# Kernel optimization log

Hardware: AMD Instinct MI355X
Metric: run time of the kernel (lower is better)

The kernel has to match this reference:

```python
import jax, jax.numpy as jnp
import numpy as np

B, S, D, H = 1, 3072, 2048, 16
HD = D // H          # head_dim = 128
C = HD // 2          # rotary complex pairs = 64
EPS = 1e-6
WINDOW = 3           # frames of sliding-window attention on each side
L_TOKENS = 256       # tokens per frame (forward arg L)
NUM_FRAMES = S // L_TOKENS


def setup_inputs() -> dict:
    key = jax.random.key(0)
    ks = jax.random.split(key, 5)
    scale = 1.0 / np.sqrt(D)
    x = jax.random.normal(ks[0], (B, S, D), jnp.float32)
    wq = jax.random.normal(ks[1], (D, D), jnp.float32) * scale
    wk = jax.random.normal(ks[2], (D, D), jnp.float32) * scale
    wv = jax.random.normal(ks[3], (D, D), jnp.float32) * scale
    wo = jax.random.normal(ks[4], (D, D), jnp.float32) * scale
    bq = jnp.zeros((D,), jnp.float32)
    bk = jnp.zeros((D,), jnp.float32)
    bv = jnp.zeros((D,), jnp.float32)
    bo = jnp.zeros((D,), jnp.float32)
    gq = jnp.ones((D,), jnp.float32)
    gk = jnp.ones((D,), jnp.float32)
    # rotary freqs as cos/sin of angle t * theta_c (source uses a complex [S,1,C] tensor)
    t = jnp.arange(S, dtype=jnp.float32)
    inv_freq = 1.0 / (10000.0 ** (jnp.arange(C, dtype=jnp.float32) / C))
    ang = t[:, None] * inv_freq[None, :]        # [S, C]
    cos = jnp.cos(ang)[:, None, :]              # [S, 1, C]
    sin = jnp.sin(ang)[:, None, :]              # [S, 1, C]
    return {"x": x, "wq": wq, "bq": bq, "wk": wk, "bk": bk, "wv": wv,
            "bv": bv, "wo": wo, "bo": bo, "gq": gq, "gk": gk,
            "cos": cos, "sin": sin, "f": NUM_FRAMES, "L": L_TOKENS}


def _rms_norm(h, g, eps=EPS):
    # tensor_parallel_rms_norm with tp_size=1: fp32 variance, rsqrt, scale by weight
    hf = h.astype(jnp.float32)
    var = jnp.mean(hf * hf, axis=-1, keepdims=True)
    return (hf * jax.lax.rsqrt(var + eps) * g).astype(h.dtype)


def _rope(h, cos, sin):
    # complex rotation on interleaved (real, imag) pairs per head (rope_apply_for3d)
    b, s, d = h.shape
    hd = 2 * cos.shape[-1]
    n = d // hd
    hr = h.reshape(b, s, n, hd)
    xr, xi = hr[..., 0::2], hr[..., 1::2]       # [b,s,n,C]
    c, sn = cos[None], sin[None]                # [1,s,1,C] broadcast over heads
    yr = xr * c - xi * sn
    yi = xr * sn + xi * c
    y = jnp.stack([yr, yi], axis=-1).reshape(b, s, n, hd)
    return y.reshape(b, s, d)


def reference(x, wq, bq, wk, bk, wv, bv, wo, bo, gq, gk, cos, sin, f, L):
    q = _rope(_rms_norm(x @ wq.T + bq, gq), cos, sin)
    k = _rope(_rms_norm(x @ wk.T + bk, gk), cos, sin)
    v = x @ wv.T + bv
    b, s, d = q.shape
    hd = 2 * cos.shape[-1]
    n = d // hd
    qh = q.reshape(b, s, n, hd)
    kh = k.reshape(b, s, n, hd)
    vh = v.reshape(b, s, n, hd)
    scale = 1.0 / np.sqrt(hd)
    scores = jnp.einsum('bqnd,bknd->bnqk', qh, kh) * scale
    win = L * WINDOW
    idx = jnp.arange(s)
    delta = idx[None, :] - idx[:, None]
    mask = (delta <= win) & (delta >= -win)
    scores = jnp.where(mask[None, None], scores, -jnp.inf)
    probs = jax.nn.softmax(scores, axis=-1)
    out = jnp.einsum('bnqk,bknd->bqnd', probs, vh).reshape(b, s, d)
    return out @ wo.T + bo
```

## Files before the change

kernel.cpp:

```cpp
#include <hip/hip_runtime.h>
#include <stdint.h>

typedef unsigned short u16;
typedef __attribute__((ext_vector_type(8))) short short8;
typedef __attribute__((ext_vector_type(4))) float f32x4;

#define S_LEN 3072
#define D_DIM 2048
#define WIN 768
#define INV_SQRT_HD 0.08838834764831845f
#define M_SHIFT 12.0f

__device__ __forceinline__ u16 f2bf(float x) {
  union { float f; uint32_t u; } v; v.f = x;
  uint32_t r = v.u + 0x7FFFu + ((v.u >> 16) & 1u);
  return (u16)(r >> 16);
}
__device__ __forceinline__ float bf2f(u16 x) {
  union { uint32_t u; float f; } v; v.u = ((uint32_t)x) << 16;
  return v.f;
}

__device__ __forceinline__ void load_lds16(const void* g, void* l) {
  __builtin_amdgcn_global_load_lds(
      (const __attribute__((address_space(1))) void*)g,
      (__attribute__((address_space(3))) void*)l, 16, 0, 0);
}

#define MFMA16(a, b, c) __builtin_amdgcn_mfma_f32_16x16x32_bf16((a), (b), (c), 0, 0, 0)

__global__ __launch_bounds__(256) void k_cvt_all(const float* __restrict__ x,
                                                 const float* __restrict__ w0, const float* __restrict__ w1,
                                                 const float* __restrict__ w2, const float* __restrict__ w3,
                                                 const float* __restrict__ bq, const float* __restrict__ bk,
                                                 const float* __restrict__ bv,
                                                 u16* __restrict__ xo,
                                                 u16* __restrict__ o0, u16* __restrict__ o1,
                                                 u16* __restrict__ o2, u16* __restrict__ o3,
                                                 float* __restrict__ bias_all,
                                                 int n4x, int n4w) {
  int i = blockIdx.x * 256 + threadIdx.x;
  if (i < n4x + 4 * n4w) {
    const float* in;
    u16* out;
    int off;
    if (i < n4x) {
      in = x; out = xo; off = i;
    } else {
      int j = i - n4x;
      int seg = j / n4w;
      off = j - seg * n4w;
      in = seg == 0 ? w0 : seg == 1 ? w1 : seg == 2 ? w2 : w3;
      out = seg == 0 ? o0 : seg == 1 ? o1 : seg == 2 ? o2 : o3;
    }
    float4 v = ((const float4*)in)[off];
    ushort4 o;
    o.x = f2bf(v.x); o.y = f2bf(v.y); o.z = f2bf(v.z); o.w = f2bf(v.w);
    ((ushort4*)out)[off] = o;
  } else {
    int j = i - n4x - 4 * n4w;
    int seg = j >> 9, off = j & 511;
    const float* in = seg == 0 ? bq : seg == 1 ? bk : bv;
    ((float4*)bias_all)[j] = ((const float4*)in)[off];
  }
}

__global__ __launch_bounds__(256, 3) void k_gemm_qkv(const u16* __restrict__ A,
                                                     const u16* __restrict__ Ball,
                                                     const float* __restrict__ bias_all,
                                                     u16* __restrict__ QKV) {
  __shared__ u16 lA[128 * 32];
  __shared__ u16 lB[192 * 32];
  const int id = blockIdx.x;
  const int xcd = id & 7, local = id >> 3;
  const int m_idx = xcd * 3 + local / 32;
  const int n_idx = local % 32;
  const int m0 = m_idx * 128;
  const int n0g = n_idx * 192;
  const int t = threadIdx.x;
  const int lane = t & 63, w = t >> 6, lo = lane & 15, g = lane >> 4;
  const int wr = w >> 1, wc = w & 1;

  const int srow = t >> 2;
  const int sch = (t & 3) ^ ((srow ^ (srow >> 3)) & 3);
  const u16* ga = A + (size_t)(m0 + srow) * D_DIM + sch * 8;
  const u16* gb = Ball + (size_t)(n0g + srow) * D_DIM + sch * 8;

  const f32x4 zero4 = {0.f, 0.f, 0.f, 0.f};
  f32x4 acc[4][6];
#pragma unroll
  for (int m = 0; m < 4; ++m)
#pragma unroll
    for (int n = 0; n < 6; ++n) acc[m][n] = zero4;

  for (int k0 = 0; k0 < D_DIM; k0 += 32) {
    load_lds16(ga + k0, &lA[t * 8]);
    load_lds16(ga + (size_t)64 * D_DIM + k0, &lA[2048 + t * 8]);
    load_lds16(gb + k0, &lB[t * 8]);
    load_lds16(gb + (size_t)64 * D_DIM + k0, &lB[2048 + t * 8]);
    load_lds16(gb + (size_t)128 * D_DIM + k0, &lB[4096 + t * 8]);
    __syncthreads();
    short8 af[4], bfr[6];
#pragma unroll
    for (int m = 0; m < 4; ++m) {
      const int R = wr * 64 + m * 16 + lo;
      af[m] = *(const short8*)&lA[R * 32 + ((g ^ ((R ^ (R >> 3)) & 3)) << 3)];
    }
#pragma unroll
    for (int n = 0; n < 6; ++n) {
      const int R = wc * 96 + n * 16 + lo;
      bfr[n] = *(const short8*)&lB[R * 32 + ((g ^ ((R ^ (R >> 3)) & 3)) << 3)];
    }
#pragma unroll
    for (int m = 0; m < 4; ++m)
#pragma unroll
      for (int n = 0; n < 6; ++n) acc[m][n] = MFMA16(af[m], bfr[n], acc[m][n]);
    __syncthreads();
  }

#pragma unroll
  for (int m = 0; m < 4; ++m) {
    const int row = m0 + wr * 64 + m * 16 + 4 * g;
#pragma unroll
    for (int n = 0; n < 6; ++n) {
      const int col_g = n0g + wc * 96 + n * 16 + lo;
      const int seg_c = col_g >> 11, c = col_g & 2047;
      u16* D = QKV + (size_t)seg_c * S_LEN * D_DIM;
      const float bb = bias_all[col_g];
#pragma unroll
      for (int r = 0; r < 4; ++r)
        D[(size_t)(row + r) * D_DIM + c] = f2bf(acc[m][n][r] + bb);
    }
  }
}

__device__ __forceinline__ void gemm_body(const u16* __restrict__ A, const u16* __restrict__ B,
                                          int m0, int n0, int t, f32x4 (*acc)[4],
                                          u16* lA, u16* lB) {
  const int lane = t & 63, w = t >> 6, lo = lane & 15, g = lane >> 4;
  const int wr = w >> 1, wc = w & 1;
  const int srow = t >> 2;
  const int sch = (t & 3) ^ ((srow ^ (srow >> 3)) & 3);
  const u16* ga = A + (size_t)(m0 + srow) * D_DIM + sch * 8;
  const u16* gb = B + (size_t)(n0 + srow) * D_DIM + sch * 8;
  for (int k0 = 0; k0 < D_DIM; k0 += 32) {
    load_lds16(ga + k0, &lA[t * 8]);
    load_lds16(ga + (size_t)64 * D_DIM + k0, &lA[2048 + t * 8]);
    load_lds16(gb + k0, &lB[t * 8]);
    load_lds16(gb + (size_t)64 * D_DIM + k0, &lB[2048 + t * 8]);
    __syncthreads();
    short8 af[4], bfr[4];
#pragma unroll
    for (int m = 0; m < 4; ++m) {
      const int R = wr * 64 + m * 16 + lo;
      af[m] = *(const short8*)&lA[R * 32 + ((g ^ ((R ^ (R >> 3)) & 3)) << 3)];
    }
#pragma unroll
    for (int n = 0; n < 4; ++n) {
      const int R = wc * 64 + n * 16 + lo;
      bfr[n] = *(const short8*)&lB[R * 32 + ((g ^ ((R ^ (R >> 3)) & 3)) << 3)];
    }
#pragma unroll
    for (int m = 0; m < 4; ++m)
#pragma unroll
      for (int n = 0; n < 4; ++n) acc[m][n] = MFMA16(af[m], bfr[n], acc[m][n]);
    __syncthreads();
  }
}

__global__ __launch_bounds__(256) void k_gemm_wo(const u16* __restrict__ A,
                                                 const u16* __restrict__ B,
                                                 const float* __restrict__ bias,
                                                 float* __restrict__ C) {
  __shared__ u16 lA[128 * 32];
  __shared__ u16 lB[128 * 32];
  const int id = blockIdx.x;
  const int xcd = id & 7, local = id >> 3;
  const int m_idx = xcd * 3 + local / 16;
  const int n_idx = local % 16;
  const int m0 = m_idx * 128, n0 = n_idx * 128;
  const int t = threadIdx.x;
  const int lane = t & 63, w = t >> 6, lo = lane & 15, g = lane >> 4;
  const int wr = w >> 1, wc = w & 1;
  const f32x4 zero4 = {0.f, 0.f, 0.f, 0.f};
  f32x4 acc[4][4];
#pragma unroll
  for (int m = 0; m < 4; ++m)
#pragma unroll
    for (int n = 0; n < 4; ++n) acc[m][n] = zero4;
  gemm_body(A, B, m0, n0, t, acc, lA, lB);
#pragma unroll
  for (int m = 0; m < 4; ++m) {
    const int row = m0 + wr * 64 + m * 16 + 4 * g;
#pragma unroll
    for (int n = 0; n < 4; ++n) {
      const int col = n0 + wc * 64 + n * 16 + lo;
      const float bb = bias[col];
#pragma unroll
      for (int r = 0; r < 4; ++r)
        C[(size_t)(row + r) * 2048 + col] = acc[m][n][r] + bb;
    }
  }
}

__global__ __launch_bounds__(256) void k_aux(const u16* __restrict__ Q0, const u16* __restrict__ K0,
                                             const u16* __restrict__ V0,
                                             const float* __restrict__ gq, const float* __restrict__ gk,
                                             const float* __restrict__ cosT, const float* __restrict__ sinT,
                                             u16* __restrict__ qo, u16* __restrict__ ko,
                                             u16* __restrict__ vT) {
  const int bid = blockIdx.x, t = threadIdx.x;
  if (bid < 2 * S_LEN) {
    const int s = bid >> 1, which = bid & 1;
    const u16* H = which ? K0 : Q0;
    const float* gain = which ? gk : gq;
    u16* out = which ? ko : qo;
    const short8 hv = *(const short8*)(H + (size_t)s * D_DIM + t * 8);
    float h[8];
#pragma unroll
    for (int j = 0; j < 8; ++j) h[j] = bf2f((u16)hv[j]);
    float ss = 0.f;
#pragma unroll
    for (int j = 0; j < 8; ++j) ss += h[j] * h[j];
#pragma unroll
    for (int off = 32; off > 0; off >>= 1) ss += __shfl_xor(ss, off);
    __shared__ float red[4];
    if ((t & 63) == 0) red[t >> 6] = ss;
    __syncthreads();
    ss = red[0] + red[1] + red[2] + red[3];
    const float rs = rsqrtf(ss * (1.f / D_DIM) + 1e-6f);
    const float4 g0 = *(const float4*)(gain + t * 8);
    const float4 g1 = *(const float4*)(gain + t * 8 + 4);
    float y[8];
    y[0] = h[0] * rs * g0.x; y[1] = h[1] * rs * g0.y;
    y[2] = h[2] * rs * g0.z; y[3] = h[3] * rs * g0.w;
    y[4] = h[4] * rs * g1.x; y[5] = h[5] * rs * g1.y;
    y[6] = h[6] * rs * g1.z; y[7] = h[7] * rs * g1.w;
    const int cbase = ((t * 8) & 127) >> 1;
    short8 o8;
#pragma unroll
    for (int i = 0; i < 4; ++i) {
      const float cs = cosT[s * 64 + cbase + i];
      const float sn = sinT[s * 64 + cbase + i];
      const float yr = y[2 * i] * cs - y[2 * i + 1] * sn;
      const float yi = y[2 * i] * sn + y[2 * i + 1] * cs;
      o8[2 * i] = (short)f2bf(yr);
      o8[2 * i + 1] = (short)f2bf(yi);
    }
    *(short8*)(out + (size_t)s * D_DIM + t * 8) = o8;
  } else {
    __shared__ u16 tile[64][72];
    const int idx = bid - 2 * S_LEN;
    const int s0 = (idx % 48) * 64, d0 = (idx / 48) * 64;
    const int r = t >> 3, c8 = (t & 7) * 8;
#pragma unroll
    for (int p = 0; p < 2; ++p) {
      short8 v = *(const short8*)&V0[(size_t)(s0 + r + p * 32) * D_DIM + d0 + c8];
#pragma unroll
      for (int j = 0; j < 8; ++j) tile[r + p * 32][c8 + j] = (u16)v[j];
    }
    __syncthreads();
#pragma unroll
    for (int p = 0; p < 2; ++p) {
      const int dr = r + p * 32;
      short8 o;
#pragma unroll
      for (int j = 0; j < 8; ++j) o[j] = (short)tile[c8 + j][dr];
      *(short8*)&vT[(size_t)(d0 + dr) * S_LEN + s0 + c8] = o;
    }
  }
}

__global__ __launch_bounds__(256, 3) void k_attn5(const u16* __restrict__ Q,
                                                  const u16* __restrict__ Kmat,
                                                  const u16* __restrict__ Vt,
                                                  u16* __restrict__ Oa,
                                                  u16* __restrict__ Ob,
                                                  float* __restrict__ lbuf) {
  const int id = blockIdx.x;
  const int xcd = id & 7, local = id >> 3;
  const int h = xcd * 2 + (local / 48);
  const int rr_ = local % 48;
  const int qt = rr_ >> 1, z = rr_ & 1;
  const int t = threadIdx.x, w = t >> 6, lane = t & 63, lo = lane & 15, g = lane >> 4;
  const int q0 = qt * 128;
  const int wrow = q0 + w * 32;
  const size_t hoff = (size_t)h * 128;

  __shared__ u16 lK[2][32 * 128];
  __shared__ u16 lV[2][128 * 32];
  __shared__ u16 ldsp[4][32][40];

  short8 qf[2][4];
#pragma unroll
  for (int m = 0; m < 2; ++m) {
    const u16* qp = Q + (size_t)(wrow + m * 16 + lo) * D_DIM + hoff + g * 8;
#pragma unroll
    for (int c = 0; c < 4; ++c) qf[m][c] = *(const short8*)(qp + c * 32);
  }

  const f32x4 zero4 = {0.f, 0.f, 0.f, 0.f};
  f32x4 oacc[2][8];
#pragma unroll
  for (int m = 0; m < 2; ++m)
#pragma unroll
    for (int ct = 0; ct < 8; ++ct) oacc[m][ct] = zero4;
  float lrun[2][4] = {{0.f, 0.f, 0.f, 0.f}, {0.f, 0.f, 0.f, 0.f}};

  int jlo = q0 - WIN; if (jlo < 0) jlo = 0;
  int jhi = q0 + 127 + WIN + 1; if (jhi > S_LEN) jhi = S_LEN;
  const int NT = (jhi - jlo) >> 5;
  const int it0 = z * (NT >> 1), it1 = it0 + (NT >> 1);

  const int krow = t >> 4,          kch  = (t & 15) ^ (krow & 7);
  const int krow1 = (t + 256) >> 4, kch1 = (t & 15) ^ (krow1 & 7);
  const int vrow = t >> 2,          vch  = (t & 3) ^ ((vrow >> 1) & 3);
  const int vrow1 = (t + 256) >> 2, vch1 = (t & 3) ^ ((vrow1 >> 1) & 3);

#define STAGE5(buf, jj)                                                                              \
  do {                                                                                               \
    load_lds16(Kmat + (size_t)((jj) + krow) * D_DIM + hoff + (kch << 3), &lK[buf][t * 8]);           \
    load_lds16(Kmat + (size_t)((jj) + krow1) * D_DIM + hoff + (kch1 << 3), &lK[buf][(t + 256) * 8]); \
    load_lds16(Vt + (size_t)(hoff + vrow) * S_LEN + (jj) + (vch << 3), &lV[buf][t * 8]);             \
    load_lds16(Vt + (size_t)(hoff + vrow1) * S_LEN + (jj) + (vch1 << 3), &lV[buf][(t + 256) * 8]);   \
  } while (0)

  STAGE5(0, jlo + (it0 << 5));
  __syncthreads();
  int cur = 0;
  for (int it = it0; it < it1; ++it) {
    const int j0 = jlo + (it << 5);
    if (it + 1 < it1) STAGE5(cur ^ 1, j0 + 32);

    f32x4 sc[2][2];
    sc[0][0] = zero4; sc[0][1] = zero4; sc[1][0] = zero4; sc[1][1] = zero4;
#pragma unroll
    for (int half = 0; half < 2; ++half) {
#pragma unroll
      for (int c = 0; c < 4; ++c) {
        const short8 kf = *(const short8*)
            &lK[cur][(half * 16 + lo) * 128 + (((g + 4 * c) ^ (lo & 7)) << 3)];
        sc[0][half] = MFMA16(qf[0][c], kf, sc[0][half]);
        sc[1][half] = MFMA16(qf[1][c], kf, sc[1][half]);
      }
    }

    const int dq = j0 - q0;
    const bool interior = (dq >= -640) && (dq <= 736);
#pragma unroll
    for (int m = 0; m < 2; ++m) {
#pragma unroll
      for (int r = 0; r < 4; ++r) {
        float a0 = fmaf(sc[m][0][r], INV_SQRT_HD, -M_SHIFT);
        float a1 = fmaf(sc[m][1][r], INV_SQRT_HD, -M_SHIFT);
        if (!interior) {
          const int dk = j0 + lo - (wrow + m * 16 + 4 * g + r);
          if (dk < -WIN || dk > WIN) a0 = -3e38f;
          if (dk + 16 < -WIN || dk + 16 > WIN) a1 = -3e38f;
        }
        const float p0 = __expf(a0);
        const float p1 = __expf(a1);
        lrun[m][r] += p0 + p1;
        ldsp[w][m * 16 + 4 * g + r][lo] = f2bf(p0);
        ldsp[w][m * 16 + 4 * g + r][16 + lo] = f2bf(p1);
      }
    }

    const short8 pf0 = *(const short8*)&ldsp[w][lo][g * 8];
    const short8 pf1 = *(const short8*)&ldsp[w][16 + lo][g * 8];
#pragma unroll
    for (int ct = 0; ct < 8; ++ct) {
      const short8 vf = *(const short8*)
          &lV[cur][(ct * 16 + lo) * 32 + ((g ^ ((lo >> 1) & 3)) << 3)];
      oacc[0][ct] = MFMA16(pf0, vf, oacc[0][ct]);
      oacc[1][ct] = MFMA16(pf1, vf, oacc[1][ct]);
    }
    __syncthreads();
    cur ^= 1;
  }
#undef STAGE5

#pragma unroll
  for (int off = 8; off > 0; off >>= 1)
#pragma unroll
    for (int m = 0; m < 2; ++m)
#pragma unroll
      for (int r = 0; r < 4; ++r) lrun[m][r] += __shfl_xor(lrun[m][r], off);

  u16* Op = z ? Ob : Oa;
#pragma unroll
  for (int m = 0; m < 2; ++m)
#pragma unroll
    for (int r = 0; r < 4; ++r) {
      const int row = wrow + m * 16 + 4 * g + r;
#pragma unroll
      for (int ct = 0; ct < 8; ++ct)
        Op[(size_t)row * D_DIM + hoff + ct * 16 + lo] = f2bf(oacc[m][ct][r]);
      if (lo == 0) lbuf[(size_t)z * S_LEN * 16 + (size_t)row * 16 + h] = lrun[m][r];
    }
}

__global__ __launch_bounds__(256) void k_combine(const u16* __restrict__ Oa,
                                                 const u16* __restrict__ Ob,
                                                 const float* __restrict__ lbuf,
                                                 u16* __restrict__ out) {
  const int i = blockIdx.x * 256 + threadIdx.x;
  const int s = i >> 8, d8 = (i & 255) * 8, h = d8 >> 7;
  const float la = lbuf[(size_t)s * 16 + h];
  const float lb = lbuf[(size_t)S_LEN * 16 + (size_t)s * 16 + h];
  const float inv = 1.f / (la + lb);
  const size_t base = (size_t)s * D_DIM + d8;
  const short8 a = *(const short8*)(Oa + base);
  const short8 b = *(const short8*)(Ob + base);
  short8 o;
#pragma unroll
  for (int j = 0; j < 8; ++j)
    o[j] = (short)f2bf((bf2f((u16)a[j]) + bf2f((u16)b[j])) * inv);
  *(short8*)(out + base) = o;
}

extern "C" void kernel_launch(void* const* d_in, const int* in_sizes, int n_in,
                              void* d_out, int out_size, void* d_ws, size_t ws_size,
                              hipStream_t stream) {
  const float* x    = (const float*)d_in[0];
  const float* wq   = (const float*)d_in[1];
  const float* bq   = (const float*)d_in[2];
  const float* wk   = (const float*)d_in[3];
  const float* bk   = (const float*)d_in[4];
  const float* wv   = (const float*)d_in[5];
  const float* bv   = (const float*)d_in[6];
  const float* wo   = (const float*)d_in[7];
  const float* bo   = (const float*)d_in[8];
  const float* gq   = (const float*)d_in[9];
  const float* gk   = (const float*)d_in[10];
  const float* cosT = (const float*)d_in[11];
  const float* sinT = (const float*)d_in[12];

  char* ws = (char*)d_ws;
  const size_t WB = (size_t)D_DIM * D_DIM * 2;
  const size_t XB = (size_t)S_LEN * D_DIM * 2;
  u16*   wq_bf = (u16*)(ws);
  u16*   wk_bf = (u16*)(ws + WB);
  u16*   wv_bf = (u16*)(ws + 2 * WB);
  u16*   wo_bf = (u16*)(ws + 3 * WB);
  u16*   x_bf  = (u16*)(ws + 4 * WB);
  u16*   Q0b   = (u16*)(ws + 4 * WB + XB);
  u16*   K0b   = (u16*)(ws + 4 * WB + 2 * XB);
  u16*   V0b   = (u16*)(ws + 4 * WB + 3 * XB);
  float* lbuf  = (float*)(ws + 4 * WB + 4 * XB);
  float* bias_all = (float*)(ws + 4 * WB + 4 * XB + 512 * 1024);
  u16* q_bf = x_bf;
  u16* k_bf = wq_bf;
  u16* vT   = (u16*)(ws + XB);
  u16* Ob   = K0b;
  u16* Oa   = (u16*)d_out;
  u16* attn = V0b;

  const int nw4 = (D_DIM * D_DIM) / 4;
  const int nx4 = (S_LEN * D_DIM) / 4;
  const int ncvt = nx4 + 4 * nw4 + 6144 / 4;
  k_cvt_all<<<ncvt / 256, 256, 0, stream>>>(
      x, wq, wk, wv, wo, bq, bk, bv, x_bf, wq_bf, wk_bf, wv_bf, wo_bf, bias_all, nx4, nw4);

  k_gemm_qkv<<<768, 256, 0, stream>>>(x_bf, wq_bf, bias_all, Q0b);

  k_aux<<<2 * S_LEN + 1536, 256, 0, stream>>>(Q0b, K0b, V0b, gq, gk, cosT, sinT, q_bf, k_bf, vT);

  k_attn5<<<768, 256, 0, stream>>>(q_bf, k_bf, vT, Oa, Ob, lbuf);
  k_combine<<<(S_LEN * D_DIM / 8) / 256, 256, 0, stream>>>(Oa, Ob, lbuf, attn);

  k_gemm_wo<<<384, 256, 0, stream>>>(attn, wo_bf, bo, (float*)d_out);
}
```

Baseline: 221.6 us.

## Fuse Q RMS-norm/RoPE into attention and split-combine into WO GEMM

The QKV GEMM epilogue now accumulates per-row sum of squares for Q with atomics, so the Q RMS-norm and rotary are applied inside the attention kernel when it loads Q fragments. The aux kernel then only processes K and the V transpose. The separate combine kernel is removed: the WO GEMM reads both partial attention outputs, normalizes them by the summed softmax denominators, and writes the bf16 A tile into LDS directly. This saves two passes over S×D activations and one launch. In exchange, the WO A-operand loads become synchronous register loads with extra ALU work, and the Q sum of squares uses fp32 atomics whose order is nondeterministic.

```diff
diff --git a/kernel.cpp b/kernel.cpp
--- a/kernel.cpp
+++ b/kernel.cpp
@@ -38,6 +38,7 @@
                                                  u16* __restrict__ o0, u16* __restrict__ o1,
                                                  u16* __restrict__ o2, u16* __restrict__ o3,
                                                  float* __restrict__ bias_all,
+                                                 float* __restrict__ ssqQ,
                                                  int n4x, int n4w) {
   int i = blockIdx.x * 256 + threadIdx.x;
   if (i < n4x + 4 * n4w) {
@@ -59,16 +60,22 @@
     ((ushort4*)out)[off] = o;
   } else {
     int j = i - n4x - 4 * n4w;
-    int seg = j >> 9, off = j & 511;
-    const float* in = seg == 0 ? bq : seg == 1 ? bk : bv;
-    ((float4*)bias_all)[j] = ((const float4*)in)[off];
+    if (j < 1536) {
+      int seg = j >> 9, off = j & 511;
+      const float* in = seg == 0 ? bq : seg == 1 ? bk : bv;
+      ((float4*)bias_all)[j] = ((const float4*)in)[off];
+    } else {
+      float4 z = {0.f, 0.f, 0.f, 0.f};
+      ((float4*)ssqQ)[j - 1536] = z;
+    }
   }
 }
 
 __global__ __launch_bounds__(256, 3) void k_gemm_qkv(const u16* __restrict__ A,
                                                      const u16* __restrict__ Ball,
                                                      const float* __restrict__ bias_all,
-                                                     u16* __restrict__ QKV) {
+                                                     u16* __restrict__ QKV,
+                                                     float* __restrict__ ssqQ) {
   __shared__ u16 lA[128 * 32];
   __shared__ u16 lB[192 * 32];
   const int id = blockIdx.x;
@@ -118,6 +125,12 @@
     __syncthreads();
   }
 
+  float pss[4][4];
+#pragma unroll
+  for (int m = 0; m < 4; ++m)
+#pragma unroll
+    for (int r = 0; r < 4; ++r) pss[m][r] = 0.f;
+
 #pragma unroll
   for (int m = 0; m < 4; ++m) {
     const int row = m0 + wr * 64 + m * 16 + 4 * g;
@@ -128,94 +141,34 @@
       u16* D = QKV + (size_t)seg_c * S_LEN * D_DIM;
       const float bb = bias_all[col_g];
 #pragma unroll
+      for (int r = 0; r < 4; ++r) {
+        const float val = acc[m][n][r] + bb;
+        D[(size_t)(row + r) * D_DIM + c] = f2bf(val);
+        if (seg_c == 0) pss[m][r] += val * val;
+      }
+    }
+  }
+  if (n0g < 2048) {
+#pragma unroll
+    for (int m = 0; m < 4; ++m) {
+      const int row = m0 + wr * 64 + m * 16 + 4 * g;
+#pragma unroll
       for (int r = 0; r < 4; ++r)
-        D[(size_t)(row + r) * D_DIM + c] = f2bf(acc[m][n][r] + bb);
-    }
-  }
-}
-
-__device__ __forceinline__ void gemm_body(const u16* __restrict__ A, const u16* __restrict__ B,
-                                          int m0, int n0, int t, f32x4 (*acc)[4],
-                                          u16* lA, u16* lB) {
-  const int lane = t & 63, w = t >> 6, lo = lane & 15, g = lane >> 4;
-  const int wr = w >> 1, wc = w & 1;
-  const int srow = t >> 2;
-  const int sch = (t & 3) ^ ((srow ^ (srow >> 3)) & 3);
-  const u16* ga = A + (size_t)(m0 + srow) * D_DIM + sch * 8;
-  const u16* gb = B + (size_t)(n0 + srow) * D_DIM + sch * 8;
-  for (int k0 = 0; k0 < D_DIM; k0 += 32) {
-    load_lds16(ga + k0, &lA[t * 8]);
-    load_lds16(ga + (size_t)64 * D_DIM + k0, &lA[2048 + t * 8]);
-    load_lds16(gb + k0, &lB[t * 8]);
-    load_lds16(gb + (size_t)64 * D_DIM + k0, &lB[2048 + t * 8]);
-    __syncthreads();
-    short8 af[4], bfr[4];
-#pragma unroll
-    for (int m = 0; m < 4; ++m) {
-      const int R = wr * 64 + m * 16 + lo;
-      af[m] = *(const short8*)&lA[R * 32 + ((g ^ ((R ^ (R >> 3)) & 3)) << 3)];
-    }
-#pragma unroll
-    for (int n = 0; n < 4; ++n) {
-      const int R = wc * 64 + n * 16 + lo;
-      bfr[n] = *(const short8*)&lB[R * 32 + ((g ^ ((R ^ (R >> 3)) & 3)) << 3)];
-    }
-#pragma unroll
-    for (int m = 0; m < 4; ++m)
-#pragma unroll
-      for (int n = 0; n < 4; ++n) acc[m][n] = MFMA16(af[m], bfr[n], acc[m][n]);
-    __syncthreads();
-  }
-}
-
-__global__ __launch_bounds__(256) void k_gemm_wo(const u16* __restrict__ A,
-                                                 const u16* __restrict__ B,
-                                                 const float* __restrict__ bias,
-                                                 float* __restrict__ C) {
-  __shared__ u16 lA[128 * 32];
-  __shared__ u16 lB[128 * 32];
-  const int id = blockIdx.x;
-  const int xcd = id & 7, local = id >> 3;
-  const int m_idx = xcd * 3 + local / 16;
-  const int n_idx = local % 16;
-  const int m0 = m_idx * 128, n0 = n_idx * 128;
-  const int t = threadIdx.x;
-  const int lane = t & 63, w = t >> 6, lo = lane & 15, g = lane >> 4;
-  const int wr = w >> 1, wc = w & 1;
-  const f32x4 zero4 = {0.f, 0.f, 0.f, 0.f};
-  f32x4 acc[4][4];
-#pragma unroll
-  for (int m = 0; m < 4; ++m)
-#pragma unroll
-    for (int n = 0; n < 4; ++n) acc[m][n] = zero4;
-  gemm_body(A, B, m0, n0, t, acc, lA, lB);
-#pragma unroll
-  for (int m = 0; m < 4; ++m) {
-    const int row = m0 + wr * 64 + m * 16 + 4 * g;
-#pragma unroll
-    for (int n = 0; n < 4; ++n) {
-      const int col = n0 + wc * 64 + n * 16 + lo;
-      const float bb = bias[col];
-#pragma unroll
-      for (int r = 0; r < 4; ++r)
-        C[(size_t)(row + r) * 2048 + col] = acc[m][n][r] + bb;
-    }
-  }
-}
-
-__global__ __launch_bounds__(256) void k_aux(const u16* __restrict__ Q0, const u16* __restrict__ K0,
+        if (pss[m][r] != 0.f) atomicAdd(&ssqQ[row + r], pss[m][r]);
+    }
+  }
+}
+
+__global__ __launch_bounds__(256) void k_aux(const u16* __restrict__ K0,
                                              const u16* __restrict__ V0,
-                                             const float* __restrict__ gq, const float* __restrict__ gk,
+                                             const float* __restrict__ gk,
                                              const float* __restrict__ cosT, const float* __restrict__ sinT,
-                                             u16* __restrict__ qo, u16* __restrict__ ko,
+                                             u16* __restrict__ ko,
                                              u16* __restrict__ vT) {
   const int bid = blockIdx.x, t = threadIdx.x;
-  if (bid < 2 * S_LEN) {
-    const int s = bid >> 1, which = bid & 1;
-    const u16* H = which ? K0 : Q0;
-    const float* gain = which ? gk : gq;
-    u16* out = which ? ko : qo;
-    const short8 hv = *(const short8*)(H + (size_t)s * D_DIM + t * 8);
+  if (bid < S_LEN) {
+    const int s = bid;
+    const short8 hv = *(const short8*)(K0 + (size_t)s * D_DIM + t * 8);
     float h[8];
 #pragma unroll
     for (int j = 0; j < 8; ++j) h[j] = bf2f((u16)hv[j]);
@@ -229,8 +182,8 @@
     __syncthreads();
     ss = red[0] + red[1] + red[2] + red[3];
     const float rs = rsqrtf(ss * (1.f / D_DIM) + 1e-6f);
-    const float4 g0 = *(const float4*)(gain + t * 8);
-    const float4 g1 = *(const float4*)(gain + t * 8 + 4);
+    const float4 g0 = *(const float4*)(gk + t * 8);
+    const float4 g1 = *(const float4*)(gk + t * 8 + 4);
     float y[8];
     y[0] = h[0] * rs * g0.x; y[1] = h[1] * rs * g0.y;
     y[2] = h[2] * rs * g0.z; y[3] = h[3] * rs * g0.w;
@@ -247,10 +200,10 @@
       o8[2 * i] = (short)f2bf(yr);
       o8[2 * i + 1] = (short)f2bf(yi);
     }
-    *(short8*)(out + (size_t)s * D_DIM + t * 8) = o8;
+    *(short8*)(ko + (size_t)s * D_DIM + t * 8) = o8;
   } else {
     __shared__ u16 tile[64][72];
-    const int idx = bid - 2 * S_LEN;
+    const int idx = bid - S_LEN;
     const int s0 = (idx % 48) * 64, d0 = (idx / 48) * 64;
     const int r = t >> 3, c8 = (t & 7) * 8;
 #pragma unroll
@@ -271,7 +224,11 @@
   }
 }
 
-__global__ __launch_bounds__(256, 3) void k_attn5(const u16* __restrict__ Q,
+__global__ __launch_bounds__(256, 3) void k_attn5(const u16* __restrict__ Q0,
+                                                  const float* __restrict__ ssqQ,
+                                                  const float* __restrict__ gq,
+                                                  const float* __restrict__ cosT,
+                                                  const float* __restrict__ sinT,
                                                   const u16* __restrict__ Kmat,
                                                   const u16* __restrict__ Vt,
                                                   u16* __restrict__ Oa,
@@ -294,9 +251,30 @@
   short8 qf[2][4];
 #pragma unroll
   for (int m = 0; m < 2; ++m) {
-    const u16* qp = Q + (size_t)(wrow + m * 16 + lo) * D_DIM + hoff + g * 8;
-#pragma unroll
-    for (int c = 0; c < 4; ++c) qf[m][c] = *(const short8*)(qp + c * 32);
+    const int row = wrow + m * 16 + lo;
+    const float rs = rsqrtf(ssqQ[row] * (1.f / D_DIM) + 1e-6f);
+    const u16* qp = Q0 + (size_t)row * D_DIM + hoff + g * 8;
+#pragma unroll
+    for (int c = 0; c < 4; ++c) {
+      const short8 hv = *(const short8*)(qp + c * 32);
+      const float4 g0 = *(const float4*)(gq + hoff + c * 32 + g * 8);
+      const float4 g1 = *(const float4*)(gq + hoff + c * 32 + g * 8 + 4);
+      float y[8];
+      y[0] = bf2f((u16)hv[0]) * rs * g0.x; y[1] = bf2f((u16)hv[1]) * rs * g0.y;
+      y[2] = bf2f((u16)hv[2]) * rs * g0.z; y[3] = bf2f((u16)hv[3]) * rs * g0.w;
+      y[4] = bf2f((u16)hv[4]) * rs * g1.x; y[5] = bf2f((u16)hv[5]) * rs * g1.y;
+      y[6] = bf2f((u16)hv[6]) * rs * g1.z; y[7] = bf2f((u16)hv[7]) * rs * g1.w;
+      const int cb2 = c * 16 + g * 4;
+      short8 o;
+#pragma unroll
+      for (int i = 0; i < 4; ++i) {
+        const float cs = cosT[row * 64 + cb2 + i];
+        const float sn = sinT[row * 64 + cb2 + i];
+        o[2 * i]     = (short)f2bf(y[2 * i] * cs - y[2 * i + 1] * sn);
+        o[2 * i + 1] = (short)f2bf(y[2 * i] * sn + y[2 * i + 1] * cs);
+      }
+      qf[m][c] = o;
+    }
   }
 
   const f32x4 zero4 = {0.f, 0.f, 0.f, 0.f};
@@ -400,23 +378,84 @@
     }
 }
 
-__global__ __launch_bounds__(256) void k_combine(const u16* __restrict__ Oa,
+__global__ __launch_bounds__(256) void k_gemm_wo(const u16* __restrict__ Oa,
                                                  const u16* __restrict__ Ob,
                                                  const float* __restrict__ lbuf,
-                                                 u16* __restrict__ out) {
-  const int i = blockIdx.x * 256 + threadIdx.x;
-  const int s = i >> 8, d8 = (i & 255) * 8, h = d8 >> 7;
-  const float la = lbuf[(size_t)s * 16 + h];
-  const float lb = lbuf[(size_t)S_LEN * 16 + (size_t)s * 16 + h];
-  const float inv = 1.f / (la + lb);
-  const size_t base = (size_t)s * D_DIM + d8;
-  const short8 a = *(const short8*)(Oa + base);
-  const short8 b = *(const short8*)(Ob + base);
-  short8 o;
-#pragma unroll
-  for (int j = 0; j < 8; ++j)
-    o[j] = (short)f2bf((bf2f((u16)a[j]) + bf2f((u16)b[j])) * inv);
-  *(short8*)(out + base) = o;
+                                                 const u16* __restrict__ B,
+                                                 const float* __restrict__ bias,
+                                                 float* __restrict__ C) {
+  __shared__ u16 lA[128 * 32];
+  __shared__ u16 lB[128 * 32];
+  const int id = blockIdx.x;
+  const int xcd = id & 7, local = id >> 3;
+  const int m_idx = xcd * 3 + local / 16;
+  const int n_idx = local % 16;
+  const int m0 = m_idx * 128, n0 = n_idx * 128;
+  const int t = threadIdx.x;
+  const int lane = t & 63, w = t >> 6, lo = lane & 15, g = lane >> 4;
+  const int wr = w >> 1, wc = w & 1;
+  const int srow = t >> 2;
+  const int sch = (t & 3) ^ ((srow ^ (srow >> 3)) & 3);
+  const int row0 = m0 + srow, row1 = row0 + 64;
+  const size_t aoff0 = (size_t)row0 * D_DIM + sch * 8;
+  const size_t aoff1 = (size_t)row1 * D_DIM + sch * 8;
+  const u16* gb = B + (size_t)(n0 + srow) * D_DIM + sch * 8;
+
+  const f32x4 zero4 = {0.f, 0.f, 0.f, 0.f};
+  f32x4 acc[4][4];
+#pragma unroll
+  for (int m = 0; m < 4; ++m)
+#pragma unroll
+    for (int n = 0; n < 4; ++n) acc[m][n] = zero4;
+
+  for (int k0 = 0; k0 < D_DIM; k0 += 32) {
+    load_lds16(gb + k0, &lB[t * 8]);
+    load_lds16(gb + (size_t)64 * D_DIM + k0, &lB[2048 + t * 8]);
+    const int hh = k0 >> 7;
+    const float inv0 = 1.f / (lbuf[row0 * 16 + hh] + lbuf[(size_t)S_LEN * 16 + row0 * 16 + hh]);
+    const float inv1 = 1.f / (lbuf[row1 * 16 + hh] + lbuf[(size_t)S_LEN * 16 + row1 * 16 + hh]);
+    const short8 a0 = *(const short8*)(Oa + aoff0 + k0);
+    const short8 b0 = *(const short8*)(Ob + aoff0 + k0);
+    const short8 a1 = *(const short8*)(Oa + aoff1 + k0);
+    const short8 b1 = *(const short8*)(Ob + aoff1 + k0);
+    short8 s0, s1;
+#pragma unroll
+    for (int j = 0; j < 8; ++j) {
+      s0[j] = (short)f2bf((bf2f((u16)a0[j]) + bf2f((u16)b0[j])) * inv0);
+      s1[j] = (short)f2bf((bf2f((u16)a1[j]) + bf2f((u16)b1[j])) * inv1);
+    }
+    *(short8*)&lA[t * 8] = s0;
+    *(short8*)&lA[2048 + t * 8] = s1;
+    __syncthreads();
+    short8 af[4], bfr[4];
+#pragma unroll
+    for (int m = 0; m < 4; ++m) {
+      const int R = wr * 64 + m * 16 + lo;
+      af[m] = *(const short8*)&lA[R * 32 + ((g ^ ((R ^ (R >> 3)) & 3)) << 3)];
+    }
+#pragma unroll
+    for (int n = 0; n < 4; ++n) {
+      const int R = wc * 64 + n * 16 + lo;
+      bfr[n] = *(const short8*)&lB[R * 32 + ((g ^ ((R ^ (R >> 3)) & 3)) << 3)];
+    }
+#pragma unroll
+    for (int m = 0; m < 4; ++m)
+#pragma unroll
+      for (int n = 0; n < 4; ++n) acc[m][n] = MFMA16(af[m], bfr[n], acc[m][n]);
+    __syncthreads();
+  }
+#pragma unroll
+  for (int m = 0; m < 4; ++m) {
+    const int row = m0 + wr * 64 + m * 16 + 4 * g;
+#pragma unroll
+    for (int n = 0; n < 4; ++n) {
+      const int col = n0 + wc * 64 + n * 16 + lo;
+      const float bb = bias[col];
+#pragma unroll
+      for (int r = 0; r < 4; ++r)
+        C[(size_t)(row + r) * 2048 + col] = acc[m][n][r] + bb;
+    }
+  }
 }
 
 extern "C" void kernel_launch(void* const* d_in, const int* in_sizes, int n_in,
@@ -447,27 +486,25 @@
   u16*   Q0b   = (u16*)(ws + 4 * WB + XB);
   u16*   K0b   = (u16*)(ws + 4 * WB + 2 * XB);
   u16*   V0b   = (u16*)(ws + 4 * WB + 3 * XB);
-  float* lbuf  = (float*)(ws + 4 * WB + 4 * XB);
+  float* lbuf     = (float*)(ws + 4 * WB + 4 * XB);
   float* bias_all = (float*)(ws + 4 * WB + 4 * XB + 512 * 1024);
-  u16* q_bf = x_bf;
+  float* ssqQ     = (float*)(ws + 4 * WB + 4 * XB + 768 * 1024);
+  u16*   Oa       = (u16*)(ws + 4 * WB + 4 * XB + 1024 * 1024);
   u16* k_bf = wq_bf;
   u16* vT   = (u16*)(ws + XB);
   u16* Ob   = K0b;
-  u16* Oa   = (u16*)d_out;
-  u16* attn = V0b;
 
   const int nw4 = (D_DIM * D_DIM) / 4;
   const int nx4 = (S_LEN * D_DIM) / 4;
-  const int ncvt = nx4 + 4 * nw4 + 6144 / 4;
+  const int ncvt = nx4 + 4 * nw4 + 1536 + 768;
   k_cvt_all<<<ncvt / 256, 256, 0, stream>>>(
-      x, wq, wk, wv, wo, bq, bk, bv, x_bf, wq_bf, wk_bf, wv_bf, wo_bf, bias_all, nx4, nw4);
-
-  k_gemm_qkv<<<768, 256, 0, stream>>>(x_bf, wq_bf, bias_all, Q0b);
-
-  k_aux<<<2 * S_LEN + 1536, 256, 0, stream>>>(Q0b, K0b, V0b, gq, gk, cosT, sinT, q_bf, k_bf, vT);
-
-  k_attn5<<<768, 256, 0, stream>>>(q_bf, k_bf, vT, Oa, Ob, lbuf);
-  k_combine<<<(S_LEN * D_DIM / 8) / 256, 256, 0, stream>>>(Oa, Ob, lbuf, attn);
-
-  k_gemm_wo<<<384, 256, 0, stream>>>(attn, wo_bf, bo, (float*)d_out);
-}
+      x, wq, wk, wv, wo, bq, bk, bv, x_bf, wq_bf, wk_bf, wv_bf, wo_bf, bias_all, ssqQ, nx4, nw4);
+
+  k_gemm_qkv<<<768, 256, 0, stream>>>(x_bf, wq_bf, bias_all, Q0b, ssqQ);
+
+  k_aux<<<S_LEN + 1536, 256, 0, stream>>>(K0b, V0b, gk, cosT, sinT, k_bf, vT);
+
+  k_attn5<<<768, 256, 0, stream>>>(Q0b, ssqQ, gq, cosT, sinT, k_bf, vT, Oa, Ob, lbuf);
+
+  k_gemm_wo<<<384, 256, 0, stream>>>(Oa, Ob, lbuf, wo_bf, bo, (float*)d_out);
+}
```

Measured after the change: 719.5 us. +224.6%, slower.
